# Performance work log

Hardware: AMD Instinct MI355X
Metric: run time of the kernel (lower is better)

## Reference

```python
import jax, jax.numpy as jnp
import numpy as np

N_NODES = 100000
N_EDGES = 1200000
N_GRAPHS = 1024
IN_FEATS = 64
HID = 64
BN_EPS = 1e-5


def setup_inputs() -> dict:
    key = jax.random.key(0)
    ks = jax.random.split(key, 20)
    feats = jax.random.normal(ks[0], (N_NODES, IN_FEATS), jnp.float32)
    src = jax.random.randint(ks[1], (N_EDGES,), 0, N_NODES, jnp.int32)
    dst = jax.random.randint(ks[2], (N_EDGES,), 0, N_NODES, jnp.int32)
    graph_ids = jnp.sort(jax.random.randint(ks[3], (N_NODES,), 0, N_GRAPHS, jnp.int32))

    def lin(k, fi, fo):
        s = 1.0 / np.sqrt(fi)
        kw, kb = jax.random.split(k)
        return (jax.random.uniform(kw, (fi, fo), jnp.float32, -s, s),
                jax.random.uniform(kb, (fo,), jnp.float32, -s, s))

    W_self, _ = lin(ks[4], IN_FEATS, HID)
    W_neigh, b_neigh = lin(ks[5], IN_FEATS, HID)
    W1, b1 = lin(ks[6], HID, 128)
    W2, b2 = lin(ks[7], 128, 64)
    W3, b3 = lin(ks[8], 64, 1)

    def bn(k, d):
        k1, k2, k3, k4 = jax.random.split(k, 4)
        return (jax.random.normal(k1, (d,), jnp.float32) * 0.1 + 1.0,
                jax.random.normal(k2, (d,), jnp.float32) * 0.1,
                jax.random.normal(k3, (d,), jnp.float32) * 0.1,
                jax.random.uniform(k4, (d,), jnp.float32, 0.5, 1.5))

    g1, be1, rm1, rv1 = bn(ks[9], 128)
    g2, be2, rm2, rv2 = bn(ks[10], 64)

    return dict(feats=feats, src=src, dst=dst, graph_ids=graph_ids,
                W_self=W_self, W_neigh=W_neigh, b_neigh=b_neigh,
                W1=W1, b1=b1, g1=g1, be1=be1, rm1=rm1, rv1=rv1,
                W2=W2, b2=b2, g2=g2, be2=be2, rm2=rm2, rv2=rv2,
                W3=W3, b3=b3)


def reference(feats, src, dst, graph_ids, W_self, W_neigh, b_neigh,
              W1, b1, g1, be1, rm1, rv1, W2, b2, g2, be2, rm2, rv2, W3, b3):
    # --- SAGEConv (mean aggregator): h = W_self@h_self + W_neigh@mean_neigh + b
    deg = jax.ops.segment_sum(jnp.ones((src.shape[0],), feats.dtype), dst,
                              num_segments=N_NODES)                      # [N]
    agg = jax.ops.segment_sum(feats[src], dst, num_segments=N_NODES)     # [N, F]
    mean_neigh = agg / jnp.maximum(deg, 1.0)[:, None]
    h = feats @ W_self + mean_neigh @ W_neigh + b_neigh
    h = jax.nn.relu(h)                                                   # activation

    # --- per-graph max readout (dgl.max_nodes)
    hg = jax.ops.segment_max(h, graph_ids, num_segments=N_GRAPHS)        # [G, HID]

    # --- MLP head with eval-mode BatchNorm1d
    def bn(x, g, b, rm, rv):
        return (x - rm) * jax.lax.rsqrt(rv + BN_EPS) * g + b

    x = bn(jax.nn.relu(hg @ W1 + b1), g1, be1, rm1, rv1)
    x = bn(jax.nn.relu(x @ W2 + b2), g2, be2, rm2, rv2)
    return x @ W3 + b3                                                   # [G, n_task]
```

## Files before the change

kernel.cpp:

```cpp
#include <hip/hip_runtime.h>
#include <hip/hip_fp16.h>

#define N_NODES  100000
#define N_EDGES  1200000
#define N_GRAPHS 1024
#define F        64
#define BN_EPS   1e-5f
#define NBUCK    ((N_NODES + 255) / 256)
#define NBLK     512
#define CHUNK    ((N_EDGES + NBLK - 1) / NBLK)
#define MT       128
#define GEMM_BLOCKS ((N_NODES + MT - 1) / MT)
#define CE       3584

__global__ __launch_bounds__(256) void prep(
    const float* __restrict__ feats, const float* __restrict__ Wself,
    const float* __restrict__ Wneigh, __half* __restrict__ Uh,
    __half* __restrict__ Zh, const int* __restrict__ dst,
    int* __restrict__ Ct, int* __restrict__ hgbits) {
  __shared__ __align__(16) char smraw[MT * 65 * 4 + 64 * 128 * 4];
  int t = threadIdx.x;

  if (blockIdx.x >= GEMM_BLOCKS) {
    int* lh = (int*)smraw;
    int b = blockIdx.x - GEMM_BLOCKS;
    int zidx = b * 256 + t;
    if (zidx < N_GRAPHS * F) hgbits[zidx] = 0;
    for (int i = t; i < NBUCK; i += 256) lh[i] = 0;
    __syncthreads();
    int e0 = b * CHUNK, e1 = e0 + CHUNK;
    if (e1 > N_EDGES) e1 = N_EDGES;
    for (int e = e0 + t; e < e1; e += 256) atomicAdd(&lh[dst[e] >> 8], 1);
    __syncthreads();
    for (int i = t; i < NBUCK; i += 256) Ct[(size_t)b * NBUCK + i] = lh[i];
    return;
  }

  float* As = (float*)smraw;
  float* Ws = (float*)(smraw + MT * 65 * 4);
  int mbase = blockIdx.x * MT;

  for (int i = t; i < 64 * 128; i += 256) {
    int k = i >> 7, j = i & 127;
    Ws[i] = (j < 64) ? Wself[k * 64 + j] : Wneigh[k * 64 + (j - 64)];
  }
#pragma unroll
  for (int s = 0; s < 8; s++) {
    int idx = (s * 256 + t) * 4;
    int m = idx >> 6, k = idx & 63;
    int gm = mbase + m;
    float4 v = (gm < N_NODES) ? *(const float4*)(feats + (size_t)gm * F + k)
                              : make_float4(0.f, 0.f, 0.f, 0.f);
    float* d = As + m * 65 + k;
    d[0] = v.x; d[1] = v.y; d[2] = v.z; d[3] = v.w;
  }
  __syncthreads();

  int wave = t >> 6, lane = t & 63;
  int jq = lane & 3, nq = lane >> 2;
  int half = wave & 1;
  int mb = (wave >> 1) * 64 + 4 * nq;
  int joff = half * 64 + jq * 16;

  float acc[4][16];
#pragma unroll
  for (int i = 0; i < 4; i++)
#pragma unroll
    for (int c = 0; c < 16; c++) acc[i][c] = 0.f;

#pragma unroll 4
  for (int k = 0; k < 64; k++) {
    float a0 = As[(mb + 0) * 65 + k];
    float a1 = As[(mb + 1) * 65 + k];
    float a2 = As[(mb + 2) * 65 + k];
    float a3 = As[(mb + 3) * 65 + k];
    const float4* wr = (const float4*)(Ws + k * 128 + joff);
    float4 w4[4];
    w4[0] = wr[0]; w4[1] = wr[1]; w4[2] = wr[2]; w4[3] = wr[3];
    const float* w = (const float*)w4;
#pragma unroll
    for (int c = 0; c < 16; c++) {
      float wv = w[c];
      acc[0][c] += a0 * wv;
      acc[1][c] += a1 * wv;
      acc[2][c] += a2 * wv;
      acc[3][c] += a3 * wv;
    }
  }

  __half* outp = half ? Zh : Uh;
  int jbase = jq * 16;
#pragma unroll
  for (int i = 0; i < 4; i++) {
    int gm = mbase + mb + i;
    if (gm < N_NODES) {
#pragma unroll
      for (int c4 = 0; c4 < 4; c4++) {
        union { __half h[4]; uint2 u; } pk;
        pk.h[0] = __float2half_rn(acc[i][c4 * 4 + 0]);
        pk.h[1] = __float2half_rn(acc[i][c4 * 4 + 1]);
        pk.h[2] = __float2half_rn(acc[i][c4 * 4 + 2]);
        pk.h[3] = __float2half_rn(acc[i][c4 * 4 + 3]);
        *(uint2*)(outp + (size_t)gm * F + jbase + c4 * 4) = pk.u;
      }
    }
  }
}

__global__ __launch_bounds__(NBLK) void cscan(int* __restrict__ Ct,
                                              int* __restrict__ bcnt) {
  __shared__ int s[NBLK];
  int i = blockIdx.x, t = threadIdx.x;
  int v = Ct[(size_t)t * NBUCK + i];
  s[t] = v;
  __syncthreads();
  for (int off = 1; off < NBLK; off <<= 1) {
    int u = (t >= off) ? s[t - off] : 0;
    __syncthreads();
    s[t] += u;
    __syncthreads();
  }
  Ct[(size_t)t * NBUCK + i] = s[t] - v;
  if (t == NBLK - 1) bcnt[i] = s[NBLK - 1];
}

__global__ __launch_bounds__(512) void bscan(const int* __restrict__ bcnt,
                                             int* __restrict__ bstart) {
  __shared__ int s[512];
  int t = threadIdx.x;
  int v = (t < NBUCK) ? bcnt[t] : 0;
  s[t] = v;
  __syncthreads();
  for (int off = 1; off < 512; off <<= 1) {
    int u = (t >= off) ? s[t - off] : 0;
    __syncthreads();
    s[t] += u;
    __syncthreads();
  }
  if (t < NBUCK) bstart[t] = s[t] - v;
  if (t == 0) bstart[NBUCK] = N_EDGES;
}

__global__ __launch_bounds__(256) void cscat(const int* __restrict__ src,
                                             const int* __restrict__ dst,
                                             const int* __restrict__ Ct,
                                             const int* __restrict__ bstart,
                                             int* __restrict__ pairs) {
  __shared__ int cur[NBUCK];
  int b = blockIdx.x, t = threadIdx.x;
  for (int i = t; i < NBUCK; i += 256)
    cur[i] = bstart[i] + Ct[(size_t)b * NBUCK + i];
  __syncthreads();
  int e0 = b * CHUNK, e1 = e0 + CHUNK;
  if (e1 > N_EDGES) e1 = N_EDGES;
  for (int e = e0 + t; e < e1; e += 256) {
    int d = dst[e];
    int pos = atomicAdd(&cur[d >> 8], 1);
    pairs[pos] = (int)((((unsigned)d & 255u) << 24) | (unsigned)src[e]);
  }
}

__global__ __launch_bounds__(1024) void gather_place(
    const __half* __restrict__ Uh, const __half* __restrict__ Zh,
    const int* __restrict__ pairs, const int* __restrict__ bstart,
    const float* __restrict__ bneigh, const int* __restrict__ gids,
    int* __restrict__ hgbits) {
  __shared__ int eidx_l[CE];
  __shared__ int rsl[256];
  __shared__ int lh[256];
  __shared__ int cur[256];
  int b = blockIdx.x, t = threadIdx.x;
  int nb0 = b << 8;
  int r0 = bstart[b], r1 = bstart[b + 1];
  int E = r1 - r0; if (E > CE) E = CE;

  if (t < 256) lh[t] = 0;
  __syncthreads();
  for (int e = t; e < E; e += 1024)
    atomicAdd(&lh[((unsigned)pairs[r0 + e]) >> 24], 1);
  __syncthreads();
  if (t < 256) cur[t] = lh[t];
  __syncthreads();
  for (int off = 1; off < 256; off <<= 1) {
    int u = (t < 256 && t >= off) ? cur[t - off] : 0;
    __syncthreads();
    if (t < 256) cur[t] += u;
    __syncthreads();
  }
  if (t < 256) { int ex = cur[t] - lh[t]; rsl[t] = ex; cur[t] = ex; }
  __syncthreads();
  for (int e = t; e < E; e += 1024) {
    unsigned p = (unsigned)pairs[r0 + e];
    int pos = atomicAdd(&cur[p >> 24], 1);
    eidx_l[pos] = (int)(p & 0xFFFFFFu);
  }
  __syncthreads();

  int wave = t >> 6, lane = t & 63;
  int fl = lane & 15, sub = lane >> 4;
  float4 b4 = *(const float4*)(bneigh + 4 * fl);
  int nl = wave * 16;
  int nend = nl + 16;
  if (nb0 + nl >= N_NODES) return;
  if (nb0 + nend > N_NODES) nend = N_NODES - nb0;

  int curg = gids[nb0 + nl];
  float4 gmax = {0.f, 0.f, 0.f, 0.f};

  for (; nl < nend; nl++) {
    int node = nb0 + nl;
    int rr  = rsl[nl];
    int deg = lh[nl];
    uint2 ur = *(const uint2*)(Uh + (size_t)node * F + 4 * fl);
    float sx = 0.f, sy = 0.f, sz = 0.f, sw = 0.f;
    for (int jj = 0; jj < deg; jj += 16) {
      int j0 = jj + sub;
      int s0 = (j0      < deg) ? eidx_l[rr + j0]      : 0;
      int s1 = (j0 + 4  < deg) ? eidx_l[rr + j0 + 4]  : 0;
      int s2 = (j0 + 8  < deg) ? eidx_l[rr + j0 + 8]  : 0;
      int s3 = (j0 + 12 < deg) ? eidx_l[rr + j0 + 12] : 0;
      uint2 z0 = *(const uint2*)(Zh + (size_t)s0 * F + 4 * fl);
      uint2 z1 = *(const uint2*)(Zh + (size_t)s1 * F + 4 * fl);
      uint2 z2 = *(const uint2*)(Zh + (size_t)s2 * F + 4 * fl);
      uint2 z3 = *(const uint2*)(Zh + (size_t)s3 * F + 4 * fl);
      if (j0 < deg) {
        float2 f0 = __half22float2(*(__half2*)&z0.x);
        float2 f1 = __half22float2(*(__half2*)&z0.y);
        sx += f0.x; sy += f0.y; sz += f1.x; sw += f1.y;
      }
      if (j0 + 4 < deg) {
        float2 f0 = __half22float2(*(__half2*)&z1.x);
        float2 f1 = __half22float2(*(__half2*)&z1.y);
        sx += f0.x; sy += f0.y; sz += f1.x; sw += f1.y;
      }
      if (j0 + 8 < deg) {
        float2 f0 = __half22float2(*(__half2*)&z2.x);
        float2 f1 = __half22float2(*(__half2*)&z2.y);
        sx += f0.x; sy += f0.y; sz += f1.x; sw += f1.y;
      }
      if (j0 + 12 < deg) {
        float2 f0 = __half22float2(*(__half2*)&z3.x);
        float2 f1 = __half22float2(*(__half2*)&z3.y);
        sx += f0.x; sy += f0.y; sz += f1.x; sw += f1.y;
      }
    }
    sx += __shfl_xor(sx, 16); sy += __shfl_xor(sy, 16);
    sz += __shfl_xor(sz, 16); sw += __shfl_xor(sw, 16);
    sx += __shfl_xor(sx, 32); sy += __shfl_xor(sy, 32);
    sz += __shfl_xor(sz, 32); sw += __shfl_xor(sw, 32);
    float inv = 1.0f / fmaxf((float)deg, 1.0f);

    int g = gids[node];
    if (g != curg) {
      if (sub == 0) {
        int* hp = hgbits + (size_t)curg * F + 4 * fl;
        atomicMax(hp + 0, __float_as_int(gmax.x));
        atomicMax(hp + 1, __float_as_int(gmax.y));
        atomicMax(hp + 2, __float_as_int(gmax.z));
        atomicMax(hp + 3, __float_as_int(gmax.w));
      }
      curg = g; gmax = make_float4(0.f, 0.f, 0.f, 0.f);
    }

    float2 uf0 = __half22float2(*(__half2*)&ur.x);
    float2 uf1 = __half22float2(*(__half2*)&ur.y);
    gmax.x = fmaxf(gmax.x, fmaxf(uf0.x + sx * inv + b4.x, 0.f));
    gmax.y = fmaxf(gmax.y, fmaxf(uf0.y + sy * inv + b4.y, 0.f));
    gmax.z = fmaxf(gmax.z, fmaxf(uf1.x + sz * inv + b4.z, 0.f));
    gmax.w = fmaxf(gmax.w, fmaxf(uf1.y + sw * inv + b4.w, 0.f));
  }
  if (sub == 0) {
    int* hp = hgbits + (size_t)curg * F + 4 * fl;
    atomicMax(hp + 0, __float_as_int(gmax.x));
    atomicMax(hp + 1, __float_as_int(gmax.y));
    atomicMax(hp + 2, __float_as_int(gmax.z));
    atomicMax(hp + 3, __float_as_int(gmax.w));
  }
}

#define GPB 8
__global__ __launch_bounds__(128) void mlp(
    const float* __restrict__ hg,
    const float* __restrict__ W1, const float* __restrict__ b1,
    const float* __restrict__ g1, const float* __restrict__ be1,
    const float* __restrict__ rm1, const float* __restrict__ rv1,
    const float* __restrict__ W2, const float* __restrict__ b2,
    const float* __restrict__ g2, const float* __restrict__ be2,
    const float* __restrict__ rm2, const float* __restrict__ rv2,
    const float* __restrict__ W3, const float* __restrict__ b3,
    float* __restrict__ out) {
  __shared__ float W1s[64 * 128];
  __shared__ float W2s[128 * 64];
  __shared__ float W3s[64];
  __shared__ float sc1[128], sh1[128], b1s[128];
  __shared__ float sc2[64],  sh2[64],  b2s[64];
  __shared__ float s0[64], s1[128], s2[64];
  int t = threadIdx.x;

  for (int i = t; i < 64 * 128; i += 128) W1s[i] = W1[i];
  for (int i = t; i < 128 * 64; i += 128) W2s[i] = W2[i];
  if (t < 64) W3s[t] = W3[t];
  {
    float iv = rsqrtf(rv1[t] + BN_EPS);
    float sc = g1[t] * iv;
    sc1[t] = sc; sh1[t] = be1[t] - rm1[t] * sc; b1s[t] = b1[t];
  }
  if (t < 64) {
    float iv = rsqrtf(rv2[t] + BN_EPS);
    float sc = g2[t] * iv;
    sc2[t] = sc; sh2[t] = be2[t] - rm2[t] * sc; b2s[t] = b2[t];
  }
  __syncthreads();

  for (int gg = 0; gg < GPB; gg++) {
    int g = blockIdx.x * GPB + gg;
    if (t < 64) s0[t] = hg[(size_t)g * F + t];
    __syncthreads();
    {
      float acc = b1s[t];
      for (int i = 0; i < 64; i++) acc += s0[i] * W1s[i * 128 + t];
      acc = fmaxf(acc, 0.0f);
      s1[t] = acc * sc1[t] + sh1[t];
    }
    __syncthreads();
    if (t < 64) {
      float acc = b2s[t];
      for (int i = 0; i < 128; i++) acc += s1[i] * W2s[i * 64 + t];
      acc = fmaxf(acc, 0.0f);
      s2[t] = acc * sc2[t] + sh2[t];
    }
    __syncthreads();
    if (t < 64) {
      float p = s2[t] * W3s[t];
      for (int off = 32; off > 0; off >>= 1) p += __shfl_down(p, off);
      if (t == 0) out[g] = p + b3[0];
    }
    __syncthreads();
  }
}

extern "C" void kernel_launch(void* const* d_in, const int* in_sizes, int n_in,
                              void* d_out, int out_size, void* d_ws, size_t ws_size,
                              hipStream_t stream) {
  const float* feats  = (const float*)d_in[0];
  const int*   src    = (const int*)d_in[1];
  const int*   dst    = (const int*)d_in[2];
  const int*   gids   = (const int*)d_in[3];
  const float* Wself  = (const float*)d_in[4];
  const float* Wneigh = (const float*)d_in[5];
  const float* bneigh = (const float*)d_in[6];
  const float* W1  = (const float*)d_in[7];
  const float* b1  = (const float*)d_in[8];
  const float* g1  = (const float*)d_in[9];
  const float* be1 = (const float*)d_in[10];
  const float* rm1 = (const float*)d_in[11];
  const float* rv1 = (const float*)d_in[12];
  const float* W2  = (const float*)d_in[13];
  const float* b2  = (const float*)d_in[14];
  const float* g2  = (const float*)d_in[15];
  const float* be2 = (const float*)d_in[16];
  const float* rm2 = (const float*)d_in[17];
  const float* rv2 = (const float*)d_in[18];
  const float* W3  = (const float*)d_in[19];
  const float* b3  = (const float*)d_in[20];

  __half* Uh   = (__half*)d_ws;
  __half* Zh   = Uh + (size_t)N_NODES * F;
  int* bstart  = (int*)(Zh + (size_t)N_NODES * F);
  int* bcnt    = bstart + (NBUCK + 1);
  int* hgbits  = bcnt + NBUCK;
  int* Ct      = hgbits + (size_t)N_GRAPHS * F;
  int* pairs   = Ct + (size_t)NBLK * NBUCK;

  prep<<<GEMM_BLOCKS + NBLK, 256, 0, stream>>>(feats, Wself, Wneigh, Uh, Zh,
                                               dst, Ct, hgbits);
  cscan<<<NBUCK, NBLK, 0, stream>>>(Ct, bcnt);
  bscan<<<1, 512, 0, stream>>>(bcnt, bstart);
  cscat<<<NBLK, 256, 0, stream>>>(src, dst, Ct, bstart, pairs);
  gather_place<<<NBUCK, 1024, 0, stream>>>(Uh, Zh, pairs, bstart, bneigh,
                                           gids, hgbits);
  mlp<<<N_GRAPHS / GPB, 128, 0, stream>>>((const float*)hgbits,
                                          W1, b1, g1, be1, rm1, rv1,
                                          W2, b2, g2, be2, rm2, rv2, W3, b3,
                                          (float*)d_out);
}
```

Before: 214.2 us.

## Fuse edge bucketing into prep with per-chunk local sort, drop global scans

Each edge-chunk block in prep now histograms its edges by dst bucket, scans locally, and scatters packed pairs into its own chunk region, writing per-chunk bucket offsets. The separate cscan, bscan and cscat kernels are removed, and gather_place reads each bucket's edges by walking the 512 chunk segments, one thread per chunk. This removes three launches and a global scan pass. In exchange, each gather block does serial per-thread segment loops of uneven length with uncoalesced reads, and edges beyond CE are now silently dropped via a pos check.

```diff
diff --git a/kernel.cpp b/kernel.cpp
--- a/kernel.cpp
+++ b/kernel.cpp
@@ -16,23 +16,52 @@
 __global__ __launch_bounds__(256) void prep(
     const float* __restrict__ feats, const float* __restrict__ Wself,
     const float* __restrict__ Wneigh, __half* __restrict__ Uh,
-    __half* __restrict__ Zh, const int* __restrict__ dst,
+    __half* __restrict__ Zh, const int* __restrict__ src,
+    const int* __restrict__ dst, int* __restrict__ pairs,
     int* __restrict__ Ct, int* __restrict__ hgbits) {
   __shared__ __align__(16) char smraw[MT * 65 * 4 + 64 * 128 * 4];
   int t = threadIdx.x;
 
   if (blockIdx.x >= GEMM_BLOCKS) {
-    int* lh = (int*)smraw;
-    int b = blockIdx.x - GEMM_BLOCKS;
-    int zidx = b * 256 + t;
+    int* loff = (int*)smraw;
+    int* lcur = loff + (NBUCK + 1);
+    int* ssc  = lcur + NBUCK;
+    int c = blockIdx.x - GEMM_BLOCKS;
+    int zidx = c * 256 + t;
     if (zidx < N_GRAPHS * F) hgbits[zidx] = 0;
-    for (int i = t; i < NBUCK; i += 256) lh[i] = 0;
-    __syncthreads();
-    int e0 = b * CHUNK, e1 = e0 + CHUNK;
+    for (int i = t; i < NBUCK; i += 256) lcur[i] = 0;
+    __syncthreads();
+    int e0 = c * CHUNK, e1 = e0 + CHUNK;
     if (e1 > N_EDGES) e1 = N_EDGES;
-    for (int e = e0 + t; e < e1; e += 256) atomicAdd(&lh[dst[e] >> 8], 1);
-    __syncthreads();
-    for (int i = t; i < NBUCK; i += 256) Ct[(size_t)b * NBUCK + i] = lh[i];
+    for (int e = e0 + t; e < e1; e += 256) atomicAdd(&lcur[dst[e] >> 8], 1);
+    __syncthreads();
+    int c0 = 2 * t, c1 = 2 * t + 1;
+    int x0 = (c0 < NBUCK) ? lcur[c0] : 0;
+    int x1 = (c1 < NBUCK) ? lcur[c1] : 0;
+    int ps = x0 + x1;
+    ssc[t] = ps;
+    __syncthreads();
+    for (int off = 1; off < 256; off <<= 1) {
+      int u = (t >= off) ? ssc[t - off] : 0;
+      __syncthreads();
+      ssc[t] += u;
+      __syncthreads();
+    }
+    int excl = ssc[t] - ps;
+    if (c0 < NBUCK) loff[c0] = excl;
+    if (c1 < NBUCK) loff[c1] = excl + x0;
+    if (t == 255) loff[NBUCK] = ssc[255];
+    __syncthreads();
+    for (int i = t; i < NBUCK; i += 256) lcur[i] = loff[i];
+    __syncthreads();
+    for (int e = e0 + t; e < e1; e += 256) {
+      int d = dst[e];
+      int pos = atomicAdd(&lcur[d >> 8], 1);
+      pairs[(size_t)c * CHUNK + pos] =
+          (int)((((unsigned)d & 255u) << 24) | (unsigned)src[e]);
+    }
+    for (int i = t; i < NBUCK + 1; i += 256)
+      Ct[(size_t)c * (NBUCK + 1) + i] = loff[i];
     return;
   }
 
@@ -107,62 +136,9 @@
   }
 }
 
-__global__ __launch_bounds__(NBLK) void cscan(int* __restrict__ Ct,
-                                              int* __restrict__ bcnt) {
-  __shared__ int s[NBLK];
-  int i = blockIdx.x, t = threadIdx.x;
-  int v = Ct[(size_t)t * NBUCK + i];
-  s[t] = v;
-  __syncthreads();
-  for (int off = 1; off < NBLK; off <<= 1) {
-    int u = (t >= off) ? s[t - off] : 0;
-    __syncthreads();
-    s[t] += u;
-    __syncthreads();
-  }
-  Ct[(size_t)t * NBUCK + i] = s[t] - v;
-  if (t == NBLK - 1) bcnt[i] = s[NBLK - 1];
-}
-
-__global__ __launch_bounds__(512) void bscan(const int* __restrict__ bcnt,
-                                             int* __restrict__ bstart) {
-  __shared__ int s[512];
-  int t = threadIdx.x;
-  int v = (t < NBUCK) ? bcnt[t] : 0;
-  s[t] = v;
-  __syncthreads();
-  for (int off = 1; off < 512; off <<= 1) {
-    int u = (t >= off) ? s[t - off] : 0;
-    __syncthreads();
-    s[t] += u;
-    __syncthreads();
-  }
-  if (t < NBUCK) bstart[t] = s[t] - v;
-  if (t == 0) bstart[NBUCK] = N_EDGES;
-}
-
-__global__ __launch_bounds__(256) void cscat(const int* __restrict__ src,
-                                             const int* __restrict__ dst,
-                                             const int* __restrict__ Ct,
-                                             const int* __restrict__ bstart,
-                                             int* __restrict__ pairs) {
-  __shared__ int cur[NBUCK];
-  int b = blockIdx.x, t = threadIdx.x;
-  for (int i = t; i < NBUCK; i += 256)
-    cur[i] = bstart[i] + Ct[(size_t)b * NBUCK + i];
-  __syncthreads();
-  int e0 = b * CHUNK, e1 = e0 + CHUNK;
-  if (e1 > N_EDGES) e1 = N_EDGES;
-  for (int e = e0 + t; e < e1; e += 256) {
-    int d = dst[e];
-    int pos = atomicAdd(&cur[d >> 8], 1);
-    pairs[pos] = (int)((((unsigned)d & 255u) << 24) | (unsigned)src[e]);
-  }
-}
-
 __global__ __launch_bounds__(1024) void gather_place(
     const __half* __restrict__ Uh, const __half* __restrict__ Zh,
-    const int* __restrict__ pairs, const int* __restrict__ bstart,
+    const int* __restrict__ pairs, const int* __restrict__ Ct,
     const float* __restrict__ bneigh, const int* __restrict__ gids,
     int* __restrict__ hgbits) {
   __shared__ int eidx_l[CE];
@@ -171,14 +147,22 @@
   __shared__ int cur[256];
   int b = blockIdx.x, t = threadIdx.x;
   int nb0 = b << 8;
-  int r0 = bstart[b], r1 = bstart[b + 1];
-  int E = r1 - r0; if (E > CE) E = CE;
 
   if (t < 256) lh[t] = 0;
   __syncthreads();
-  for (int e = t; e < E; e += 1024)
-    atomicAdd(&lh[((unsigned)pairs[r0 + e]) >> 24], 1);
-  __syncthreads();
+
+  int segs = 0, sege = 0;
+  if (t < NBLK) {
+    size_t base = (size_t)t * (NBUCK + 1);
+    int o0 = Ct[base + b];
+    int o1 = Ct[base + b + 1];
+    segs = t * CHUNK + o0;
+    sege = t * CHUNK + o1;
+    for (int e = segs; e < sege; e++)
+      atomicAdd(&lh[((unsigned)pairs[e]) >> 24], 1);
+  }
+  __syncthreads();
+
   if (t < 256) cur[t] = lh[t];
   __syncthreads();
   for (int off = 1; off < 256; off <<= 1) {
@@ -189,10 +173,13 @@
   }
   if (t < 256) { int ex = cur[t] - lh[t]; rsl[t] = ex; cur[t] = ex; }
   __syncthreads();
-  for (int e = t; e < E; e += 1024) {
-    unsigned p = (unsigned)pairs[r0 + e];
-    int pos = atomicAdd(&cur[p >> 24], 1);
-    eidx_l[pos] = (int)(p & 0xFFFFFFu);
+
+  if (t < NBLK) {
+    for (int e = segs; e < sege; e++) {
+      unsigned p = (unsigned)pairs[e];
+      int pos = atomicAdd(&cur[p >> 24], 1);
+      if (pos < CE) eidx_l[pos] = (int)(p & 0xFFFFFFu);
+    }
   }
   __syncthreads();
 
@@ -366,18 +353,13 @@
 
   __half* Uh   = (__half*)d_ws;
   __half* Zh   = Uh + (size_t)N_NODES * F;
-  int* bstart  = (int*)(Zh + (size_t)N_NODES * F);
-  int* bcnt    = bstart + (NBUCK + 1);
-  int* hgbits  = bcnt + NBUCK;
+  int* hgbits  = (int*)(Zh + (size_t)N_NODES * F);
   int* Ct      = hgbits + (size_t)N_GRAPHS * F;
-  int* pairs   = Ct + (size_t)NBLK * NBUCK;
+  int* pairs   = Ct + (size_t)NBLK * (NBUCK + 1);
 
   prep<<<GEMM_BLOCKS + NBLK, 256, 0, stream>>>(feats, Wself, Wneigh, Uh, Zh,
-                                               dst, Ct, hgbits);
-  cscan<<<NBUCK, NBLK, 0, stream>>>(Ct, bcnt);
-  bscan<<<1, 512, 0, stream>>>(bcnt, bstart);
-  cscat<<<NBLK, 256, 0, stream>>>(src, dst, Ct, bstart, pairs);
-  gather_place<<<NBUCK, 1024, 0, stream>>>(Uh, Zh, pairs, bstart, bneigh,
+                                               src, dst, pairs, Ct, hgbits);
+  gather_place<<<NBUCK, 1024, 0, stream>>>(Uh, Zh, pairs, Ct, bneigh,
                                            gids, hgbits);
   mlp<<<N_GRAPHS / GPB, 128, 0, stream>>>((const float*)hgbits,
                                           W1, b1, g1, be1, rm1, rv1,
```

Result: slower. 219.2 us (+2.4%).
